# Kernel tuning notes

Hardware: AMD Instinct MI355X
Metric: run time of the kernel (lower is better)

The kernel has to match this reference:

```python
import jax, jax.numpy as jnp
import numpy as np

B, S, D, H = 4, 2048, 256, 8
DH = D // H
DFF = 4 * D
EPS = 1e-5


def _layernorm(x, w, b):
    mu = jnp.mean(x, axis=-1, keepdims=True)
    var = jnp.mean((x - mu) ** 2, axis=-1, keepdims=True)
    return (x - mu) * jax.lax.rsqrt(var + EPS) * w + b


def setup_inputs() -> dict:
    key = jax.random.key(0)
    ks = jax.random.split(key, 16)
    s = 0.02
    return {
        "x": jax.random.normal(ks[0], (B, S, D), jnp.float32),
        "in_proj_w": jax.random.normal(ks[1], (3 * D, D), jnp.float32) * s,
        "in_proj_b": jax.random.normal(ks[2], (3 * D,), jnp.float32) * s,
        "out_w": jax.random.normal(ks[3], (D, D), jnp.float32) * s,
        "out_b": jax.random.normal(ks[4], (D,), jnp.float32) * s,
        "ln1_w": jnp.ones((D,), jnp.float32),
        "ln1_b": jnp.zeros((D,), jnp.float32),
        "ln2_w": jnp.ones((D,), jnp.float32),
        "ln2_b": jnp.zeros((D,), jnp.float32),
        "ff1_w": jax.random.normal(ks[5], (DFF, D), jnp.float32) * s,
        "ff1_b": jax.random.normal(ks[6], (DFF,), jnp.float32) * s,
        "ff2_w": jax.random.normal(ks[7], (D, DFF), jnp.float32) * s,
        "ff2_b": jax.random.normal(ks[8], (D,), jnp.float32) * s,
        "slopes": jax.random.normal(ks[9], (H, 1, 1), jnp.float32),
    }


def reference(x, in_proj_w, in_proj_b, out_w, out_b, ln1_w, ln1_b, ln2_w, ln2_b,
              ff1_w, ff1_b, ff2_w, ff2_b, slopes):
    # learned ALiBi-style relative bias: (H, S, S)
    pos = jnp.arange(S, dtype=jnp.float32)
    rel = jnp.abs(pos[None, :] - pos[:, None])          # (S, S)
    bias = -jnp.abs(slopes) * rel[None, :, :]           # (H, S, S)

    xn = _layernorm(x, ln1_w, ln1_b)
    qkv = jnp.einsum('bsd,ed->bse', xn, in_proj_w) + in_proj_b
    q, k, v = jnp.split(qkv, 3, axis=-1)
    # (B, H, S, DH)
    q = q.reshape(B, S, H, DH).transpose(0, 2, 1, 3)
    k = k.reshape(B, S, H, DH).transpose(0, 2, 1, 3)
    v = v.reshape(B, S, H, DH).transpose(0, 2, 1, 3)

    scores = jnp.einsum('bhqd,bhkd->bhqk', q, k) / jnp.sqrt(jnp.float32(DH))
    scores = scores + bias[None, :, :, :]
    attn = jax.nn.softmax(scores, axis=-1)
    ctx = jnp.einsum('bhqk,bhkd->bhqd', attn, v)
    ctx = ctx.transpose(0, 2, 1, 3).reshape(B, S, D)
    attn_out = jnp.einsum('bsd,ed->bse', ctx, out_w) + out_b

    x = x + attn_out
    xn2 = _layernorm(x, ln2_w, ln2_b)
    h = jnp.einsum('bsd,fd->bsf', xn2, ff1_w) + ff1_b
    h = jax.nn.gelu(h, approximate=False)
    ff_out = jnp.einsum('bsf,df->bsd', h, ff2_w) + ff2_b
    return x + ff_out
```

## Files before the change

kernel.cpp:

```cpp
#include <hip/hip_runtime.h>
#include <hip/hip_bf16.h>
#include <math.h>

#define S_LEN 2048
#define D_MODEL 256
#define N_HEADS 8
#define HEAD_DIM 32
#define D_FF 1024
#define ROWS_TOTAL 8192

typedef __attribute__((ext_vector_type(8))) short short8;
typedef __attribute__((ext_vector_type(4))) float f32x4;

__device__ inline ushort f2bf(float f) {
    unsigned u = __builtin_bit_cast(unsigned, f);
    unsigned r = (u + 0x7fffu + ((u >> 16) & 1u)) >> 16;
    return (ushort)r;
}

__device__ inline float bf2f(ushort u) {
    return __builtin_bit_cast(float, ((unsigned)u) << 16);
}

__device__ inline unsigned cvtpk(float a, float b) {
    unsigned r;
    asm("v_cvt_pk_bf16_f32 %0, %1, %2" : "=v"(r) : "v"(a), "v"(b));
    return r;
}

__global__ __launch_bounds__(256) void prep_kernel(
    const float* __restrict__ w0, ushort* __restrict__ o0,
    const float* __restrict__ x, const float* __restrict__ lnw,
    const float* __restrict__ lnb, ushort* __restrict__ xnb) {
    int blk = blockIdx.x;
    if (blk < 192) {
        int i = blk * 256 + threadIdx.x;
        float4 v = ((const float4*)w0)[i];
        ushort4 u = {f2bf(v.x), f2bf(v.y), f2bf(v.z), f2bf(v.w)};
        ((ushort4*)o0)[i] = u;
    } else {
        int wid = threadIdx.x >> 6, lane = threadIdx.x & 63;
        int row = (blk - 192) * 4 + wid;
        float4 v = ((const float4*)(x + (size_t)row * D_MODEL))[lane];
        float4 wv = ((const float4*)lnw)[lane];
        float4 bv = ((const float4*)lnb)[lane];
        float s = v.x + v.y + v.z + v.w;
        float s2 = v.x * v.x + v.y * v.y + v.z * v.z + v.w * v.w;
        #pragma unroll
        for (int off2 = 1; off2 < 64; off2 <<= 1) {
            s  += __shfl_xor(s, off2);
            s2 += __shfl_xor(s2, off2);
        }
        float mu = s * (1.0f / D_MODEL);
        float var = s2 * (1.0f / D_MODEL) - mu * mu;
        float rstd = rsqrtf(var + 1e-5f);
        ushort4 o = {f2bf((v.x - mu) * rstd * wv.x + bv.x), f2bf((v.y - mu) * rstd * wv.y + bv.y),
                     f2bf((v.z - mu) * rstd * wv.z + bv.z), f2bf((v.w - mu) * rstd * wv.w + bv.w)};
        ((ushort4*)(xnb + (size_t)row * D_MODEL))[lane] = o;
    }
}

template <int EPI>
__global__ __launch_bounds__(256) void gemm_k256(
    const ushort* __restrict__ A,
    const ushort* __restrict__ W,
    const float* __restrict__ bias,
    ushort* __restrict__ outh,
    ushort* __restrict__ qout, ushort* __restrict__ kout, ushort* __restrict__ vout,
    const float* __restrict__ cw1, ushort* __restrict__ co1,
    const float* __restrict__ cw2, ushort* __restrict__ co2,
    const float* __restrict__ cw3, ushort* __restrict__ co3,
    int N) {
    if (EPI == 0 && blockIdx.y == 6) {
        int base = blockIdx.x * 256 + threadIdx.x;
        #pragma unroll
        for (int s = 0; s < 5; s++) {
            int i = base + s * 32768;
            if (i < 147456) {
                const float* src;
                ushort* dst;
                int off;
                if (i < 16384)      { src = cw1; dst = co1; off = i; }
                else if (i < 81920) { src = cw2; dst = co2; off = i - 16384; }
                else                { src = cw3; dst = co3; off = i - 81920; }
                float4 v = ((const float4*)src)[off];
                ushort4 u = {f2bf(v.x), f2bf(v.y), f2bf(v.z), f2bf(v.w)};
                ((ushort4*)dst)[off] = u;
            }
        }
        return;
    }
    __shared__ ushort As[64 * 128];
    __shared__ ushort Bs[128 * 128];
    const int tid = threadIdx.x;
    const int lane = tid & 63, wid = tid >> 6;
    const int l15 = lane & 15, hi = lane >> 4;
    const int wr = wid >> 1, wc = wid & 1;
    const int row0 = blockIdx.x * 64, col0 = blockIdx.y * 128;

    f32x4 acc[2][4];
    #pragma unroll
    for (int m = 0; m < 2; m++)
        #pragma unroll
        for (int n = 0; n < 4; n++) acc[m][n] = (f32x4){0.f, 0.f, 0.f, 0.f};

    short8 sa[4], sb[8];
    #pragma unroll
    for (int t = 0; t < 4; t++) {
        int c = tid + t * 256;
        sa[t] = *(const short8*)(A + (size_t)(row0 + (c >> 4)) * 256 + (c & 15) * 8);
    }
    #pragma unroll
    for (int t = 0; t < 8; t++) {
        int c = tid + t * 256;
        sb[t] = *(const short8*)(W + (size_t)(col0 + (c >> 4)) * 256 + (c & 15) * 8);
    }

    for (int k0 = 0; k0 < 256; k0 += 128) {
        __syncthreads();
        #pragma unroll
        for (int t = 0; t < 4; t++) {
            int c = tid + t * 256;
            int r = c >> 4, cb = (c & 15) * 16;
            *(short8*)((char*)As + r * 256 + (cb ^ ((r & 7) << 4))) = sa[t];
        }
        #pragma unroll
        for (int t = 0; t < 8; t++) {
            int c = tid + t * 256;
            int r = c >> 4, cb = (c & 15) * 16;
            *(short8*)((char*)Bs + r * 256 + (cb ^ ((r & 7) << 4))) = sb[t];
        }
        __syncthreads();
        if (k0 == 0) {
            #pragma unroll
            for (int t = 0; t < 4; t++) {
                int c = tid + t * 256;
                sa[t] = *(const short8*)(A + (size_t)(row0 + (c >> 4)) * 256 + 128 + (c & 15) * 8);
            }
            #pragma unroll
            for (int t = 0; t < 8; t++) {
                int c = tid + t * 256;
                sb[t] = *(const short8*)(W + (size_t)(col0 + (c >> 4)) * 256 + 128 + (c & 15) * 8);
            }
        }
        #pragma unroll
        for (int ks = 0; ks < 4; ks++) {
            short8 af[2], bfr[4];
            #pragma unroll
            for (int m = 0; m < 2; m++) {
                int r = wr * 32 + m * 16 + l15;
                af[m] = *(const short8*)((char*)As + r * 256 + ((ks * 64 + hi * 16) ^ ((r & 7) << 4)));
            }
            #pragma unroll
            for (int n = 0; n < 4; n++) {
                int r = wc * 64 + n * 16 + l15;
                bfr[n] = *(const short8*)((char*)Bs + r * 256 + ((ks * 64 + hi * 16) ^ ((r & 7) << 4)));
            }
            #pragma unroll
            for (int m = 0; m < 2; m++)
                #pragma unroll
                for (int n = 0; n < 4; n++)
                    acc[m][n] = __builtin_amdgcn_mfma_f32_16x16x32_bf16(af[m], bfr[n], acc[m][n], 0, 0, 0);
        }
    }

    #pragma unroll
    for (int m = 0; m < 2; m++) {
        #pragma unroll
        for (int n = 0; n < 4; n++) {
            #pragma unroll
            for (int r = 0; r < 4; r++) {
                int row = row0 + wr * 32 + m * 16 + hi * 4 + r;
                int col = col0 + wc * 64 + n * 16 + l15;
                float val = acc[m][n][r] + bias[col];
                if (EPI == 0) {
                    int part = col >> 8;
                    int d_o = col & 255;
                    int hh = d_o >> 5, dh = d_o & 31;
                    int bbb = row >> 11, s = row & 2047;
                    size_t bhi = (size_t)bbb * N_HEADS + hh;
                    if (part == 0) {
                        qout[(bhi * S_LEN + s) * HEAD_DIM + dh] = f2bf(val * 0.2550347137f);
                    } else {
                        int tt = s >> 6, k = s & 63;
                        size_t tb = (bhi * 32 + tt) * 2048;
                        if (part == 1)
                            kout[tb + (dh >> 3) * 512 + k * 8 + (dh & 7)] = f2bf(val);
                        else
                            vout[tb + ((size_t)((k >> 5) * 4 + ((k >> 3) & 3))) * 256 + dh * 8 + (k & 7)] = f2bf(val);
                    }
                } else {
                    float g = 0.5f * val * (1.f + erff(val * 0.70710678118654752f));
                    outh[(size_t)row * N + col] = f2bf(g);
                }
            }
        }
    }
}

__global__ __launch_bounds__(256) void gemm_ff2k(
    const ushort* __restrict__ A,
    const ushort* __restrict__ W,
    const float* __restrict__ bias,
    const ushort* __restrict__ resid,
    float* __restrict__ outf) {
    __shared__ ushort As[64 * 128];
    __shared__ ushort Bs[64 * 128];
    const int tid = threadIdx.x;
    const int lane = tid & 63, wid = tid >> 6;
    const int l15 = lane & 15, hi = lane >> 4;
    const int wr = wid >> 1, wc = wid & 1;
    const int row0 = blockIdx.x * 64, col0 = blockIdx.y * 64;

    f32x4 acc[2][2];
    #pragma unroll
    for (int m = 0; m < 2; m++)
        #pragma unroll
        for (int n = 0; n < 2; n++) acc[m][n] = (f32x4){0.f, 0.f, 0.f, 0.f};

    short8 sa[4], sb[4];
    #pragma unroll
    for (int t = 0; t < 4; t++) {
        int c = tid + t * 256;
        int r = c >> 4, e = (c & 15) * 8;
        sa[t] = *(const short8*)(A + (size_t)(row0 + r) * 1024 + e);
        sb[t] = *(const short8*)(W + (size_t)(col0 + r) * 1024 + e);
    }

    for (int k0 = 0; k0 < 1024; k0 += 128) {
        __syncthreads();
        #pragma unroll
        for (int t = 0; t < 4; t++) {
            int c = tid + t * 256;
            int r = c >> 4, cb = (c & 15) * 16;
            int sw = cb ^ ((r & 7) << 4);
            *(short8*)((char*)As + r * 256 + sw) = sa[t];
            *(short8*)((char*)Bs + r * 256 + sw) = sb[t];
        }
        __syncthreads();
        if (k0 + 128 < 1024) {
            #pragma unroll
            for (int t = 0; t < 4; t++) {
                int c = tid + t * 256;
                int r = c >> 4, e = (c & 15) * 8;
                sa[t] = *(const short8*)(A + (size_t)(row0 + r) * 1024 + k0 + 128 + e);
                sb[t] = *(const short8*)(W + (size_t)(col0 + r) * 1024 + k0 + 128 + e);
            }
        }
        #pragma unroll
        for (int ks = 0; ks < 4; ks++) {
            short8 af[2], bfr[2];
            #pragma unroll
            for (int m = 0; m < 2; m++) {
                int r = wr * 32 + m * 16 + l15;
                af[m] = *(const short8*)((char*)As + r * 256 + ((ks * 64 + hi * 16) ^ ((r & 7) << 4)));
            }
            #pragma unroll
            for (int n = 0; n < 2; n++) {
                int r = wc * 32 + n * 16 + l15;
                bfr[n] = *(const short8*)((char*)Bs + r * 256 + ((ks * 64 + hi * 16) ^ ((r & 7) << 4)));
            }
            #pragma unroll
            for (int m = 0; m < 2; m++)
                #pragma unroll
                for (int n = 0; n < 2; n++)
                    acc[m][n] = __builtin_amdgcn_mfma_f32_16x16x32_bf16(af[m], bfr[n], acc[m][n], 0, 0, 0);
        }
    }

    #pragma unroll
    for (int m = 0; m < 2; m++) {
        #pragma unroll
        for (int n = 0; n < 2; n++) {
            #pragma unroll
            for (int r = 0; r < 4; r++) {
                int row = row0 + wr * 32 + m * 16 + hi * 4 + r;
                int col = col0 + wc * 32 + n * 16 + l15;
                float rv = bf2f(resid[(size_t)row * 256 + col]);
                outf[(size_t)row * 256 + col] = acc[m][n][r] + bias[col] + rv;
            }
        }
    }
}

__global__ __launch_bounds__(256) void gemm_opln(
    const ushort* __restrict__ A,
    const ushort* __restrict__ W,
    const float* __restrict__ bias,
    const float* __restrict__ residf,
    const float* __restrict__ lnw, const float* __restrict__ lnb,
    ushort* __restrict__ xnb, ushort* __restrict__ x1b) {
    __shared__ ushort As[16 * 64];
    __shared__ ushort Bs[256 * 64];
    __shared__ float red[4][16][2];
    const int tid = threadIdx.x;
    const int lane = tid & 63, wc = tid >> 6;
    const int l15 = lane & 15, hi = lane >> 4;
    const int row0 = blockIdx.x * 16;

    f32x4 acc[4];
    #pragma unroll
    for (int n = 0; n < 4; n++) acc[n] = (f32x4){0.f, 0.f, 0.f, 0.f};

    short8 sa, sb[8];
    if (tid < 128)
        sa = *(const short8*)(A + (size_t)(row0 + (tid >> 3)) * 256 + (tid & 7) * 8);
    #pragma unroll
    for (int t = 0; t < 8; t++) {
        int c = tid + t * 256;
        sb[t] = *(const short8*)(W + (size_t)(c >> 3) * 256 + (c & 7) * 8);
    }

    for (int k0 = 0; k0 < 256; k0 += 64) {
        __syncthreads();
        if (tid < 128) {
            int r = tid >> 3, cb = (tid & 7) * 16;
            *(short8*)((char*)As + r * 128 + (cb ^ ((r & 7) << 4))) = sa;
        }
        #pragma unroll
        for (int t = 0; t < 8; t++) {
            int c = tid + t * 256;
            int r = c >> 3, cb = (c & 7) * 16;
            *(short8*)((char*)Bs + r * 128 + (cb ^ ((r & 7) << 4))) = sb[t];
        }
        __syncthreads();
        if (k0 + 64 < 256) {
            if (tid < 128)
                sa = *(const short8*)(A + (size_t)(row0 + (tid >> 3)) * 256 + k0 + 64 + (tid & 7) * 8);
            #pragma unroll
            for (int t = 0; t < 8; t++) {
                int c = tid + t * 256;
                sb[t] = *(const short8*)(W + (size_t)(c >> 3) * 256 + k0 + 64 + (c & 7) * 8);
            }
        }
        #pragma unroll
        for (int ks = 0; ks < 2; ks++) {
            short8 af, bfr[4];
            {
                int r = l15;
                af = *(const short8*)((char*)As + r * 128 + ((ks * 64 + hi * 16) ^ ((r & 7) << 4)));
            }
            #pragma unroll
            for (int n = 0; n < 4; n++) {
                int r = wc * 64 + n * 16 + l15;
                bfr[n] = *(const short8*)((char*)Bs + r * 128 + ((ks * 64 + hi * 16) ^ ((r & 7) << 4)));
            }
            #pragma unroll
            for (int n = 0; n < 4; n++)
                acc[n] = __builtin_amdgcn_mfma_f32_16x16x32_bf16(af, bfr[n], acc[n], 0, 0, 0);
        }
    }

    float x1v[4][4];
    float s1[4], s2[4];
    #pragma unroll
    for (int r = 0; r < 4; r++) { s1[r] = 0.f; s2[r] = 0.f; }
    #pragma unroll
    for (int n = 0; n < 4; n++) {
        #pragma unroll
        for (int r = 0; r < 4; r++) {
            int row = row0 + hi * 4 + r;
            int col = wc * 64 + n * 16 + l15;
            float v = acc[n][r] + bias[col] + residf[(size_t)row * 256 + col];
            x1v[n][r] = v;
            s1[r] += v;
            s2[r] += v * v;
        }
    }
    #pragma unroll
    for (int r = 0; r < 4; r++) {
        #pragma unroll
        for (int off = 1; off < 16; off <<= 1) {
            s1[r] += __shfl_xor(s1[r], off);
            s2[r] += __shfl_xor(s2[r], off);
        }
    }
    if (l15 == 0) {
        #pragma unroll
        for (int r = 0; r < 4; r++) {
            red[wc][hi * 4 + r][0] = s1[r];
            red[wc][hi * 4 + r][1] = s2[r];
        }
    }
    __syncthreads();
    #pragma unroll
    for (int r = 0; r < 4; r++) {
        int rl = hi * 4 + r;
        float a1 = red[0][rl][0] + red[1][rl][0] + red[2][rl][0] + red[3][rl][0];
        float a2 = red[0][rl][1] + red[1][rl][1] + red[2][rl][1] + red[3][rl][1];
        float mu = a1 * (1.0f / 256.f);
        float var = a2 * (1.0f / 256.f) - mu * mu;
        float rstd = rsqrtf(var + 1e-5f);
        size_t row = row0 + rl;
        #pragma unroll
        for (int n = 0; n < 4; n++) {
            int col = wc * 64 + n * 16 + l15;
            float v = x1v[n][r];
            xnb[row * 256 + col] = f2bf((v - mu) * rstd * lnw[col] + lnb[col]);
            x1b[row * 256 + col] = f2bf(v);
        }
    }
}

__global__ __launch_bounds__(256) void attn_mfma(
    const ushort* __restrict__ qb, const ushort* __restrict__ kb,
    const ushort* __restrict__ vt, const float* __restrict__ slopes,
    ushort* __restrict__ ctxout) {
    __shared__ ushort plds[4][1024];
    const int tid = threadIdx.x;
    const int wid = tid >> 6, lane = tid & 63;
    const int l15 = lane & 15, hi = lane >> 4;
    const int bh = blockIdx.y, h = bh & (N_HEADS - 1), bb = bh >> 3;
    const int qt = blockIdx.x * 4 + wid;
    const int qbase = qt * 16;
    const float slope = fabsf(slopes[h]) * 1.4426950408889634f;

    const int wl = (int)fminf(2048.f, 20.f / fmaxf(slope, 1e-6f));
    const int tlo = max(0, (qbase - wl) >> 6);
    const int thi = min(31, (qbase + 15 + wl) >> 6);

    const ushort* Kg = kb + (size_t)bh * 32 * 2048;
    const ushort* Vg = vt + (size_t)bh * 32 * 2048;

    short8 qf = *(const short8*)(qb + ((size_t)bh * S_LEN + qbase + l15) * HEAD_DIM + hi * 8);

    f32x4 ctxa[2];
    ctxa[0] = (f32x4){0.f, 0.f, 0.f, 0.f};
    ctxa[1] = (f32x4){0.f, 0.f, 0.f, 0.f};
    float lsum = 0.f;

    char* pw = (char*)&plds[wid][0];
    const int bpi = lane & 0x30;
    const int wr_off = ((hi >> 1) << 8) + (l15 << 4) + ((hi & 1) << 3);
    const int rd0 = (hi << 8) + (l15 << 4);

    const float qoff = (float)(qbase + l15 - 4 * hi);

    short8 kfc[4], vfc[2][2];
    {
        const ushort* Kt = Kg + (size_t)tlo * 2048;
        const ushort* Vt = Vg + (size_t)tlo * 2048;
        #pragma unroll
        for (int c = 0; c < 4; c++)
            kfc[c] = *(const short8*)(Kt + (hi * 64 + 16 * c + l15) * 8);
        #pragma unroll
        for (int f = 0; f < 2; f++)
            #pragma unroll
            for (int dt = 0; dt < 2; dt++)
                vfc[f][dt] = *(const short8*)(Vt + ((f * 4 + hi) * 32 + dt * 16 + l15) * 8);
    }

    for (int t = tlo; t <= thi; ++t) {
        short8 kfn[4], vfn[2][2];
        if (t < thi) {
            const ushort* Kt = Kg + (size_t)(t + 1) * 2048;
            const ushort* Vt = Vg + (size_t)(t + 1) * 2048;
            #pragma unroll
            for (int c = 0; c < 4; c++)
                kfn[c] = *(const short8*)(Kt + (hi * 64 + 16 * c + l15) * 8);
            #pragma unroll
            for (int f = 0; f < 2; f++)
                #pragma unroll
                for (int dt = 0; dt < 2; dt++)
                    vfn[f][dt] = *(const short8*)(Vt + ((f * 4 + hi) * 32 + dt * 16 + l15) * 8);
        }

        const f32x4 z = {0.f, 0.f, 0.f, 0.f};
        f32x4 s[4];
        __builtin_amdgcn_s_setprio(1);
        #pragma unroll
        for (int c = 0; c < 4; c++)
            s[c] = __builtin_amdgcn_mfma_f32_16x16x32_bf16(kfc[c], qf, z, 0, 0, 0);
        __builtin_amdgcn_s_setprio(0);

        float dkt = qoff - (float)(64 * t);
        #pragma unroll
        for (int c = 0; c < 4; c++) {
            float d0 = dkt - (float)(16 * c);
            #pragma unroll
            for (int r = 0; r < 4; r++)
                s[c][r] = exp2f(fmaf(-slope, fabsf(d0 - (float)r), s[c][r]));
        }
        f32x4 t01 = s[0] + s[1], t23 = s[2] + s[3];
        f32x4 tt = t01 + t23;
        float tsum = (tt[0] + tt[1]) + (tt[2] + tt[3]);
        tsum += __shfl_xor(tsum, 16);
        tsum += __shfl_xor(tsum, 32);
        lsum += tsum;

        #pragma unroll
        for (int c = 0; c < 4; c++) {
            unsigned lo  = cvtpk(s[c][0], s[c][1]);
            unsigned hi2 = cvtpk(s[c][2], s[c][3]);
            *(unsigned long long*)(pw + (c << 9) + wr_off) =
                ((unsigned long long)hi2 << 32) | (unsigned long long)lo;
        }
        asm volatile("s_waitcnt lgkmcnt(0)" ::: "memory");
        short8 pa0 = *(const short8*)(pw + rd0);
        short8 pa1 = *(const short8*)(pw + 1024 + rd0);
        __builtin_amdgcn_s_setprio(1);
        #pragma unroll
        for (int dt = 0; dt < 2; dt++) {
            ctxa[dt] = __builtin_amdgcn_mfma_f32_16x16x32_bf16(pa0, vfc[0][dt], ctxa[dt], 0, 0, 0);
            ctxa[dt] = __builtin_amdgcn_mfma_f32_16x16x32_bf16(pa1, vfc[1][dt], ctxa[dt], 0, 0, 0);
        }
        __builtin_amdgcn_s_setprio(0);

        #pragma unroll
        for (int c = 0; c < 4; c++) kfc[c] = kfn[c];
        #pragma unroll
        for (int f = 0; f < 2; f++)
            #pragma unroll
            for (int dt = 0; dt < 2; dt++) vfc[f][dt] = vfn[f][dt];
    }
    float inv = 1.f / lsum;
    int invi = __builtin_bit_cast(int, inv);
    #pragma unroll
    for (int r = 0; r < 4; r++) {
        float ir = __builtin_bit_cast(float, __builtin_amdgcn_ds_bpermute(bpi + 4 * r, invi));
        size_t row = (size_t)bb * S_LEN + qbase + 4 * hi + r;
        #pragma unroll
        for (int dt = 0; dt < 2; dt++)
            ctxout[row * D_MODEL + h * HEAD_DIM + dt * 16 + l15] = f2bf(ctxa[dt][r] * ir);
    }
}

extern "C" void kernel_launch(void* const* d_in, const int* in_sizes, int n_in,
                              void* d_out, int out_size, void* d_ws, size_t ws_size,
                              hipStream_t stream) {
    const float* x      = (const float*)d_in[0];
    const float* in_w   = (const float*)d_in[1];
    const float* in_b   = (const float*)d_in[2];
    const float* outw   = (const float*)d_in[3];
    const float* outb   = (const float*)d_in[4];
    const float* ln1w   = (const float*)d_in[5];
    const float* ln1b   = (const float*)d_in[6];
    const float* ln2w   = (const float*)d_in[7];
    const float* ln2b   = (const float*)d_in[8];
    const float* ff1w   = (const float*)d_in[9];
    const float* ff1b   = (const float*)d_in[10];
    const float* ff2w   = (const float*)d_in[11];
    const float* ff2b   = (const float*)d_in[12];
    const float* slopes = (const float*)d_in[13];
    float* out = (float*)d_out;

    const size_t SZ = (size_t)ROWS_TOTAL * D_MODEL;
    ushort* xnb   = (ushort*)d_ws;
    ushort* ctxb  = xnb + SZ;
    ushort* qb16  = ctxb + SZ;
    ushort* kb16  = qb16 + SZ;
    ushort* vt16  = kb16 + SZ;
    ushort* hbb   = vt16 + SZ;
    ushort* wqkvb = hbb + 4 * SZ;
    ushort* woutb = wqkvb + 768 * 256;
    ushort* wff1b = woutb + 256 * 256;
    ushort* wff2b = wff1b + 1024 * 256;
    ushort* x1b   = wff2b + 256 * 1024;

    prep_kernel<<<192 + ROWS_TOTAL / 4, 256, 0, stream>>>(
        in_w, wqkvb, x, ln1w, ln1b, xnb);
    gemm_k256<0><<<dim3(ROWS_TOTAL / 64, 7), 256, 0, stream>>>(
        xnb, wqkvb, in_b, nullptr, qb16, kb16, vt16,
        outw, woutb, ff1w, wff1b, ff2w, wff2b, 768);
    attn_mfma<<<dim3(32, 32), 256, 0, stream>>>(qb16, kb16, vt16, slopes, ctxb);
    gemm_opln<<<ROWS_TOTAL / 16, 256, 0, stream>>>(
        ctxb, woutb, outb, x, ln2w, ln2b, xnb, x1b);
    gemm_k256<2><<<dim3(ROWS_TOTAL / 64, D_FF / 128), 256, 0, stream>>>(
        xnb, wff1b, ff1b, hbb, nullptr, nullptr, nullptr,
        nullptr, nullptr, nullptr, nullptr, nullptr, nullptr, 1024);
    gemm_ff2k<<<dim3(ROWS_TOTAL / 64, D_MODEL / 64), 256, 0, stream>>>(
        hbb, wff2b, ff2b, x1b, out);
}
```

Baseline: 70.40 us.

## Load GEMM tiles directly into LDS via global_load_lds instead of register staging

Replaces the register-staged global loads plus LDS stores in three GEMM kernels with direct global-to-LDS DMA loads, applying the XOR swizzle on the global source address. This removes VGPR staging and the separate ds_write instructions, lowering register pressure. In exchange the register-based prefetch of the next k-tile is dropped, so global loads no longer overlap with MFMA compute across iterations within a block.

```diff
diff --git a/kernel.cpp b/kernel.cpp
--- a/kernel.cpp
+++ b/kernel.cpp
@@ -104,45 +104,25 @@
         #pragma unroll
         for (int n = 0; n < 4; n++) acc[m][n] = (f32x4){0.f, 0.f, 0.f, 0.f};
 
-    short8 sa[4], sb[8];
-    #pragma unroll
-    for (int t = 0; t < 4; t++) {
-        int c = tid + t * 256;
-        sa[t] = *(const short8*)(A + (size_t)(row0 + (c >> 4)) * 256 + (c & 15) * 8);
-    }
-    #pragma unroll
-    for (int t = 0; t < 8; t++) {
-        int c = tid + t * 256;
-        sb[t] = *(const short8*)(W + (size_t)(col0 + (c >> 4)) * 256 + (c & 15) * 8);
-    }
-
     for (int k0 = 0; k0 < 256; k0 += 128) {
         __syncthreads();
         #pragma unroll
         for (int t = 0; t < 4; t++) {
             int c = tid + t * 256;
-            int r = c >> 4, cb = (c & 15) * 16;
-            *(short8*)((char*)As + r * 256 + (cb ^ ((r & 7) << 4))) = sa[t];
+            int r = c >> 4, col16 = (c & 15) << 4;
+            const char* src = (const char*)A + ((size_t)(row0 + r) * 256 + k0) * 2 +
+                              (col16 ^ ((r & 7) << 4));
+            __builtin_amdgcn_global_load_lds(src, As + (size_t)(t * 256 + wid * 64) * 8, 16, 0, 0);
         }
         #pragma unroll
         for (int t = 0; t < 8; t++) {
             int c = tid + t * 256;
-            int r = c >> 4, cb = (c & 15) * 16;
-            *(short8*)((char*)Bs + r * 256 + (cb ^ ((r & 7) << 4))) = sb[t];
+            int r = c >> 4, col16 = (c & 15) << 4;
+            const char* src = (const char*)W + ((size_t)(col0 + r) * 256 + k0) * 2 +
+                              (col16 ^ ((r & 7) << 4));
+            __builtin_amdgcn_global_load_lds(src, Bs + (size_t)(t * 256 + wid * 64) * 8, 16, 0, 0);
         }
         __syncthreads();
-        if (k0 == 0) {
-            #pragma unroll
-            for (int t = 0; t < 4; t++) {
-                int c = tid + t * 256;
-                sa[t] = *(const short8*)(A + (size_t)(row0 + (c >> 4)) * 256 + 128 + (c & 15) * 8);
-            }
-            #pragma unroll
-            for (int t = 0; t < 8; t++) {
-                int c = tid + t * 256;
-                sb[t] = *(const short8*)(W + (size_t)(col0 + (c >> 4)) * 256 + 128 + (c & 15) * 8);
-            }
-        }
         #pragma unroll
         for (int ks = 0; ks < 4; ks++) {
             short8 af[2], bfr[4];
@@ -218,35 +198,21 @@
         #pragma unroll
         for (int n = 0; n < 2; n++) acc[m][n] = (f32x4){0.f, 0.f, 0.f, 0.f};
 
-    short8 sa[4], sb[4];
-    #pragma unroll
-    for (int t = 0; t < 4; t++) {
-        int c = tid + t * 256;
-        int r = c >> 4, e = (c & 15) * 8;
-        sa[t] = *(const short8*)(A + (size_t)(row0 + r) * 1024 + e);
-        sb[t] = *(const short8*)(W + (size_t)(col0 + r) * 1024 + e);
-    }
-
     for (int k0 = 0; k0 < 1024; k0 += 128) {
         __syncthreads();
         #pragma unroll
         for (int t = 0; t < 4; t++) {
             int c = tid + t * 256;
-            int r = c >> 4, cb = (c & 15) * 16;
-            int sw = cb ^ ((r & 7) << 4);
-            *(short8*)((char*)As + r * 256 + sw) = sa[t];
-            *(short8*)((char*)Bs + r * 256 + sw) = sb[t];
+            int r = c >> 4, col16 = (c & 15) << 4;
+            int gc = col16 ^ ((r & 7) << 4);
+            __builtin_amdgcn_global_load_lds(
+                (const char*)A + ((size_t)(row0 + r) * 1024 + k0) * 2 + gc,
+                As + (size_t)(t * 256 + wid * 64) * 8, 16, 0, 0);
+            __builtin_amdgcn_global_load_lds(
+                (const char*)W + ((size_t)(col0 + r) * 1024 + k0) * 2 + gc,
+                Bs + (size_t)(t * 256 + wid * 64) * 8, 16, 0, 0);
         }
         __syncthreads();
-        if (k0 + 128 < 1024) {
-            #pragma unroll
-            for (int t = 0; t < 4; t++) {
-                int c = tid + t * 256;
-                int r = c >> 4, e = (c & 15) * 8;
-                sa[t] = *(const short8*)(A + (size_t)(row0 + r) * 1024 + k0 + 128 + e);
-                sb[t] = *(const short8*)(W + (size_t)(col0 + r) * 1024 + k0 + 128 + e);
-            }
-        }
         #pragma unroll
         for (int ks = 0; ks < 4; ks++) {
             short8 af[2], bfr[2];
@@ -302,37 +268,24 @@
     #pragma unroll
     for (int n = 0; n < 4; n++) acc[n] = (f32x4){0.f, 0.f, 0.f, 0.f};
 
-    short8 sa, sb[8];
-    if (tid < 128)
-        sa = *(const short8*)(A + (size_t)(row0 + (tid >> 3)) * 256 + (tid & 7) * 8);
-    #pragma unroll
-    for (int t = 0; t < 8; t++) {
-        int c = tid + t * 256;
-        sb[t] = *(const short8*)(W + (size_t)(c >> 3) * 256 + (c & 7) * 8);
-    }
-
     for (int k0 = 0; k0 < 256; k0 += 64) {
         __syncthreads();
-        if (tid < 128) {
-            int r = tid >> 3, cb = (tid & 7) * 16;
-            *(short8*)((char*)As + r * 128 + (cb ^ ((r & 7) << 4))) = sa;
+        if (wc < 2) {
+            int c = tid;
+            int r = c >> 3, col16 = (c & 7) << 4;
+            const char* src = (const char*)A + ((size_t)(row0 + r) * 256 + k0) * 2 +
+                              (col16 ^ ((r & 7) << 4));
+            __builtin_amdgcn_global_load_lds(src, As + (size_t)(wc * 64) * 8, 16, 0, 0);
         }
         #pragma unroll
         for (int t = 0; t < 8; t++) {
             int c = tid + t * 256;
-            int r = c >> 3, cb = (c & 7) * 16;
-            *(short8*)((char*)Bs + r * 128 + (cb ^ ((r & 7) << 4))) = sb[t];
+            int r = c >> 3, col16 = (c & 7) << 4;
+            const char* src = (const char*)W + ((size_t)r * 256 + k0) * 2 +
+                              (col16 ^ ((r & 7) << 4));
+            __builtin_amdgcn_global_load_lds(src, Bs + (size_t)(t * 256 + wc * 64) * 8, 16, 0, 0);
         }
         __syncthreads();
-        if (k0 + 64 < 256) {
-            if (tid < 128)
-                sa = *(const short8*)(A + (size_t)(row0 + (tid >> 3)) * 256 + k0 + 64 + (tid & 7) * 8);
-            #pragma unroll
-            for (int t = 0; t < 8; t++) {
-                int c = tid + t * 256;
-                sb[t] = *(const short8*)(W + (size_t)(c >> 3) * 256 + k0 + 64 + (c & 7) * 8);
-            }
-        }
         #pragma unroll
         for (int ks = 0; ks < 2; ks++) {
             short8 af, bfr[4];
```

Measured after the change: 71.50 us. About the same (+1.6%).
